# Kernel optimization log

Hardware: AMD Instinct MI355X
Metric: run time of the kernel (lower is better)

The kernel has to match this reference:

```python
import jax, jax.numpy as jnp
import numpy as np

B, H, S, D = 4, 16, 2048, 64


def setup_inputs() -> dict:
    key = jax.random.key(0)
    kq, kk, kv = jax.random.split(key, 3)
    Q = jax.random.normal(kq, (B, H, S, D), dtype=jnp.float32)
    K = jax.random.normal(kk, (B, H, S, D), dtype=jnp.float32)
    V = jax.random.normal(kv, (B, H, S, D), dtype=jnp.float32)
    mask = jnp.ones((1, 1, S, S), dtype=jnp.int32)
    return {"Q": Q, "K": K, "V": V, "mask": mask}


def reference(Q, K, V, mask):
    d_k = Q.shape[-1]
    scale = 1.0 / jnp.sqrt(jnp.asarray(d_k, dtype=Q.dtype))
    # [B, H, S, S] attention scores
    attn = jnp.einsum('bhqd,bhkd->bhqk', Q, K) * scale
    # mask == 0 -> -1e9 (matches torch boolean-index assignment)
    attn = jnp.where(mask == 0, jnp.asarray(-1e9, dtype=attn.dtype), attn)
    softmax_attn = jax.nn.softmax(attn, axis=-1)
    out = jnp.einsum('bhqk,bhkd->bhqd', softmax_attn, V)
    return out
```

## Files before the change

kernel.cpp:

```cpp
#include <hip/hip_runtime.h>

typedef __bf16 bf16;
typedef __attribute__((ext_vector_type(8))) __bf16 bf16x8;
typedef __attribute__((ext_vector_type(8))) ushort ushort8v;
typedef __attribute__((ext_vector_type(4))) ushort ushort4v;
typedef __attribute__((ext_vector_type(2))) uint uint2v;
typedef __attribute__((ext_vector_type(4))) float f32x4;

constexpr int S_LEN = 2048;
constexpr int DH    = 64;
constexpr int KVBLK = 64;
constexpr int NT    = S_LEN / KVBLK;
constexpr int QW    = 64;
constexpr float QSCALE = 0.125f * 1.44269504088896f;
constexpr float NEG    = -1.44269504e9f;
constexpr float THR    = 8.0f;
constexpr size_t TILE_BYTES = (size_t)KVBLK * DH * 2;
constexpr size_t KV_BYTES   = (size_t)64 * NT * TILE_BYTES;

__device__ __forceinline__ ushort bfb(float f) {
  bf16 b = (bf16)f;
  return __builtin_bit_cast(ushort, b);
}
__device__ __forceinline__ int SWZ(int row) {
  return ((row & 7) ^ ((row >> 3) & 7)) << 4;
}
__device__ __forceinline__ uint cvtpk(float lo, float hi) {
  uint r;
  asm("v_cvt_pk_bf16_f32 %0, %1, %2" : "=v"(r) : "v"(lo), "v"(hi));
  return r;
}

__global__ __launch_bounds__(256)
void mask_flags(const int* __restrict__ M, uint* __restrict__ F) {
  const int qt  = blockIdx.x;
  const int kt0 = blockIdx.y * 4;
  const int tid = threadIdx.x;
  const int r  = tid >> 2;
  const int c0 = (tid & 3) * 16;
  __shared__ int s[4];
  uint bits = 0;
  for (int i = 0; i < 4; ++i) {
    const int kt = kt0 + i;
    const int* row = M + (size_t)(qt * 64 + r) * S_LEN + kt * 64 + c0;
    int ok = 1;
#pragma unroll
    for (int j = 0; j < 4; ++j) {
      int4 v = *(const int4*)(row + j * 4);
      ok &= (v.x != 0) & (v.y != 0) & (v.z != 0) & (v.w != 0);
    }
    ok = __all(ok) ? 1 : 0;
    if ((tid & 63) == 0) s[tid >> 6] = ok;
    __syncthreads();
    if (s[0] & s[1] & s[2] & s[3]) bits |= 1u << kt;
    __syncthreads();
  }
  if (tid == 0) atomicOr(&F[qt], bits);
}

__global__ __launch_bounds__(256)
void cvt_kv(const float* __restrict__ K, const float* __restrict__ V,
            char* __restrict__ kws, char* __restrict__ vws) {
  const int t = blockIdx.x, bh = blockIdx.y, tid = threadIdx.x;
  const float* Kb = K + ((size_t)bh * S_LEN + t * KVBLK) * DH;
  const float* Vb = V + ((size_t)bh * S_LEN + t * KVBLK) * DH;
  char* kd = kws + ((size_t)bh * NT + t) * TILE_BYTES;
  char* vd = vws + ((size_t)bh * NT + t) * TILE_BYTES;

  const int kr0 = tid >> 3, kc8 = tid & 7;
#pragma unroll
  for (int h = 0; h < 2; ++h) {
    const int row = kr0 + 32 * h;
    const float* kp = Kb + (size_t)row * DH + kc8 * 8;
    float4 a = *(const float4*)kp;
    float4 b = *(const float4*)(kp + 4);
    ushort8v pk;
    pk[0]=bfb(a.x); pk[1]=bfb(a.y); pk[2]=bfb(a.z); pk[3]=bfb(a.w);
    pk[4]=bfb(b.x); pk[5]=bfb(b.y); pk[6]=bfb(b.z); pk[7]=bfb(b.w);
    *(ushort8v*)(kd + row * 128 + ((kc8 * 16) ^ SWZ(row))) = pk;
  }
  const int vr = (tid >> 4) * 4, vc = (tid & 15) * 4;
  float rr[4][4];
#pragma unroll
  for (int i = 0; i < 4; ++i)
    *(float4*)rr[i] = *(const float4*)(Vb + (size_t)(vr + i) * DH + vc);
#pragma unroll
  for (int c = 0; c < 4; ++c) {
    const int d = vc + c;
    ushort4v p4;
    p4[0]=bfb(rr[0][c]); p4[1]=bfb(rr[1][c]);
    p4[2]=bfb(rr[2][c]); p4[3]=bfb(rr[3][c]);
    *(ushort4v*)(vd + d * 128 + ((vr * 2) ^ SWZ(d))) = p4;
  }
}

__global__ __launch_bounds__(64, 2)
void attn_fwd_direct(const float* __restrict__ Q, const int* __restrict__ M,
                     const uint* __restrict__ F, const char* __restrict__ kws,
                     const char* __restrict__ vws, float* __restrict__ O)
{
  __shared__ __align__(16) uint pbw[QW * 32];

  const int lane = threadIdx.x & 63;
  const int qr   = lane & 15;
  const int kg   = lane >> 4;

  const int bid = blockIdx.x;
  const int nid = (bid & 7) * 256 + (bid >> 3);
  const int q0  = (nid & 31) * QW;
  const int bh  = nid >> 5;

  const float* Qb = Q + (size_t)bh * S_LEN * DH;
  const uint fmask = F[q0 >> 6];

  const char* kbase = kws + (size_t)bh * NT * TILE_BYTES;
  const char* vbase = vws + (size_t)bh * NT * TILE_BYTES;

  bf16x8 qf[4][2];
#pragma unroll
  for (int f = 0; f < 4; ++f) {
    const float* qp = Qb + (size_t)(q0 + f * 16 + qr) * DH + kg * 8;
#pragma unroll
    for (int ks = 0; ks < 2; ++ks) {
      float4 a = *(const float4*)(qp + ks * 32);
      float4 b = *(const float4*)(qp + ks * 32 + 4);
      bf16x8 t2;
      t2[0]=(bf16)(a.x*QSCALE); t2[1]=(bf16)(a.y*QSCALE);
      t2[2]=(bf16)(a.z*QSCALE); t2[3]=(bf16)(a.w*QSCALE);
      t2[4]=(bf16)(b.x*QSCALE); t2[5]=(bf16)(b.y*QSCALE);
      t2[6]=(bf16)(b.z*QSCALE); t2[7]=(bf16)(b.w*QSCALE);
      qf[f][ks] = t2;
    }
  }

  f32x4 acc[4][4];
#pragma unroll
  for (int f = 0; f < 4; ++f)
#pragma unroll
    for (int nt = 0; nt < 4; ++nt) { f32x4 z = {0.f,0.f,0.f,0.f}; acc[f][nt] = z; }
  float mrow[4] = {-1e30f,-1e30f,-1e30f,-1e30f};
  float rsum[4] = {0.f,0.f,0.f,0.f};

  int lofs[4][2];
#pragma unroll
  for (int x = 0; x < 4; ++x) {
    const int row = 16 * x + qr;
    const int sw  = SWZ(row);
#pragma unroll
    for (int ks = 0; ks < 2; ++ks)
      lofs[x][ks] = row * 128 + ((kg * 16 + 64 * ks) ^ sw);
  }
  const int psw = (qr & 7) << 4;

  for (int t = 0; t < NT; ++t) {
    const char* kt = kbase + (size_t)t * TILE_BYTES;
    const char* vt = vbase + (size_t)t * TILE_BYTES;

    f32x4 sc[4][4];
#pragma unroll
    for (int f = 0; f < 4; ++f)
#pragma unroll
      for (int ct = 0; ct < 4; ++ct) { f32x4 z = {0.f,0.f,0.f,0.f}; sc[f][ct] = z; }

    __builtin_amdgcn_s_setprio(1);
#pragma unroll
    for (int ct = 0; ct < 4; ++ct)
#pragma unroll
      for (int ks = 0; ks < 2; ++ks) {
        bf16x8 kf = *(const bf16x8*)(kt + lofs[ct][ks]);
        sc[0][ct] = __builtin_amdgcn_mfma_f32_16x16x32_bf16(kf, qf[0][ks], sc[0][ct], 0,0,0);
        sc[1][ct] = __builtin_amdgcn_mfma_f32_16x16x32_bf16(kf, qf[1][ks], sc[1][ct], 0,0,0);
        sc[2][ct] = __builtin_amdgcn_mfma_f32_16x16x32_bf16(kf, qf[2][ks], sc[2][ct], 0,0,0);
        sc[3][ct] = __builtin_amdgcn_mfma_f32_16x16x32_bf16(kf, qf[3][ks], sc[3][ct], 0,0,0);
      }
    __builtin_amdgcn_s_setprio(0);

    bf16x8 vfr[4][2];
#pragma unroll
    for (int nt = 0; nt < 4; ++nt)
#pragma unroll
      for (int ks = 0; ks < 2; ++ks)
        vfr[nt][ks] = *(const bf16x8*)(vt + lofs[nt][ks]);

    const bool allset = ((fmask >> t) & 1u) != 0u;

#pragma unroll
    for (int f = 0; f < 4; ++f) {
      if (!allset) {
        const size_t mo = (size_t)(q0 + f * 16 + qr) * S_LEN + t * KVBLK + 4 * kg;
#pragma unroll
        for (int ct = 0; ct < 4; ++ct)
#pragma unroll
          for (int r = 0; r < 4; ++r)
            if (M[mo + 16 * ct + r] == 0) sc[f][ct][r] = NEG;
      }

      float a0 = fmaxf(fmaxf(sc[f][0][0], sc[f][0][1]), sc[f][0][2]);
      float a1 = fmaxf(fmaxf(sc[f][0][3], sc[f][1][0]), sc[f][1][1]);
      float a2 = fmaxf(fmaxf(sc[f][1][2], sc[f][1][3]), sc[f][2][0]);
      float a3 = fmaxf(fmaxf(sc[f][2][1], sc[f][2][2]), sc[f][2][3]);
      float a4 = fmaxf(fmaxf(sc[f][3][0], sc[f][3][1]), sc[f][3][2]);
      float lm = fmaxf(fmaxf(a0, a1), a2);
      lm = fmaxf(fmaxf(lm, a3), a4);
      lm = fmaxf(lm, sc[f][3][3]);
      lm = fmaxf(lm, __shfl_xor(lm, 16));
      lm = fmaxf(lm, __shfl_xor(lm, 32));

      if (!__all(lm - mrow[f] <= THR)) {
        const float mnew = fmaxf(mrow[f], lm);
        const float corr = __builtin_amdgcn_exp2f(mrow[f] - mnew);
        rsum[f] *= corr;
#pragma unroll
        for (int nt = 0; nt < 4; ++nt) acc[f][nt] *= corr;
        mrow[f] = mnew;
      }

      float p[4][4];
      float ps = 0.f;
#pragma unroll
      for (int ct = 0; ct < 4; ++ct)
#pragma unroll
        for (int r = 0; r < 4; ++r) {
          p[ct][r] = __builtin_amdgcn_exp2f(sc[f][ct][r] - mrow[f]);
          ps += p[ct][r];
        }
      rsum[f] += ps;

      char* pb = (char*)pbw + (f * 16 + qr) * 128;
#pragma unroll
      for (int ct = 0; ct < 4; ++ct) {
        uint2v d2;
        d2[0] = cvtpk(p[ct][0], p[ct][1]);
        d2[1] = cvtpk(p[ct][2], p[ct][3]);
        *(uint2v*)(pb + ((32 * ct + 8 * kg) ^ psw)) = d2;
      }
    }

    __builtin_amdgcn_s_setprio(1);
#pragma unroll
    for (int ks = 0; ks < 2; ++ks) {
      bf16x8 pf0 = *(const bf16x8*)((char*)pbw + (0 * 16 + qr) * 128 + ((kg * 16 + 64 * ks) ^ psw));
      bf16x8 pf1 = *(const bf16x8*)((char*)pbw + (1 * 16 + qr) * 128 + ((kg * 16 + 64 * ks) ^ psw));
      bf16x8 pf2 = *(const bf16x8*)((char*)pbw + (2 * 16 + qr) * 128 + ((kg * 16 + 64 * ks) ^ psw));
      bf16x8 pf3 = *(const bf16x8*)((char*)pbw + (3 * 16 + qr) * 128 + ((kg * 16 + 64 * ks) ^ psw));
#pragma unroll
      for (int nt = 0; nt < 4; ++nt) {
        bf16x8 vf = vfr[nt][ks];
        acc[0][nt] = __builtin_amdgcn_mfma_f32_16x16x32_bf16(vf, pf0, acc[0][nt], 0,0,0);
        acc[1][nt] = __builtin_amdgcn_mfma_f32_16x16x32_bf16(vf, pf1, acc[1][nt], 0,0,0);
        acc[2][nt] = __builtin_amdgcn_mfma_f32_16x16x32_bf16(vf, pf2, acc[2][nt], 0,0,0);
        acc[3][nt] = __builtin_amdgcn_mfma_f32_16x16x32_bf16(vf, pf3, acc[3][nt], 0,0,0);
      }
    }
    __builtin_amdgcn_s_setprio(0);
  }

#pragma unroll
  for (int f = 0; f < 4; ++f) {
    float rs = rsum[f];
    rs += __shfl_xor(rs, 16);
    rs += __shfl_xor(rs, 32);
    const float inv = 1.0f / rs;
    float* Ob = O + ((size_t)bh * S_LEN + q0 + f * 16 + qr) * DH;
#pragma unroll
    for (int nt = 0; nt < 4; ++nt) {
      float4 o = { acc[f][nt][0] * inv, acc[f][nt][1] * inv,
                   acc[f][nt][2] * inv, acc[f][nt][3] * inv };
      *(float4*)(Ob + 16 * nt + 4 * kg) = o;
    }
  }
}

__global__ __launch_bounds__(256, 4)
void attn_fwd_fb(const float* __restrict__ Q, const float* __restrict__ K,
                 const float* __restrict__ V, const int* __restrict__ M,
                 float* __restrict__ O)
{
  __shared__ __align__(16) ushort kb[KVBLK * DH];
  __shared__ __align__(16) ushort vb[DH * KVBLK];
  __shared__ __align__(16) uint   pbw[4 * 32 * 32];

  const int tid  = threadIdx.x;
  const int lane = tid & 63;
  const int w    = tid >> 6;
  const int qr   = lane & 15;
  const int kg   = lane >> 4;

  const int flat = blockIdx.y * gridDim.x + blockIdx.x;
  const int nid  = (flat & 7) * 128 + (flat >> 3);
  const int q0   = (nid & 15) * 128;
  const int bh   = nid >> 4;

  const float* Qb = Q + ((size_t)bh * S_LEN) * DH;
  const float* Kb = K + ((size_t)bh * S_LEN) * DH;
  const float* Vb = V + ((size_t)bh * S_LEN) * DH;

  bf16x8 qf[2][2];
#pragma unroll
  for (int f = 0; f < 2; ++f) {
    const float* qp = Qb + (size_t)(q0 + w * 32 + f * 16 + qr) * DH + kg * 8;
#pragma unroll
    for (int ks = 0; ks < 2; ++ks) {
      float4 a = *(const float4*)(qp + ks * 32);
      float4 b = *(const float4*)(qp + ks * 32 + 4);
      bf16x8 t2;
      t2[0]=(bf16)(a.x*QSCALE); t2[1]=(bf16)(a.y*QSCALE);
      t2[2]=(bf16)(a.z*QSCALE); t2[3]=(bf16)(a.w*QSCALE);
      t2[4]=(bf16)(b.x*QSCALE); t2[5]=(bf16)(b.y*QSCALE);
      t2[6]=(bf16)(b.z*QSCALE); t2[7]=(bf16)(b.w*QSCALE);
      qf[f][ks] = t2;
    }
  }

  f32x4 acc[2][4];
#pragma unroll
  for (int f = 0; f < 2; ++f)
#pragma unroll
    for (int nt = 0; nt < 4; ++nt) { f32x4 z = {0.f,0.f,0.f,0.f}; acc[f][nt] = z; }
  float mrow[2] = {-1e30f, -1e30f};
  float rsum[2] = {0.f, 0.f};

  int lofs[4][2];
#pragma unroll
  for (int x = 0; x < 4; ++x) {
    const int row = 16 * x + qr;
    const int sw  = SWZ(row);
#pragma unroll
    for (int ks = 0; ks < 2; ++ks)
      lofs[x][ks] = row * 128 + ((kg * 16 + 64 * ks) ^ sw);
  }
  char* pb0 = (char*)pbw + (w * 32 + qr) * 128;
  char* pb1 = pb0 + 16 * 128;
  const int psw = (qr & 7) << 4;

  const int kr0 = tid >> 3, kc8 = tid & 7;
  const int vr = (tid >> 4) * 4, vc = (tid & 15) * 4;

  for (int t = 0; t < NT; ++t) {
    const int kv0 = t * KVBLK;
#pragma unroll
    for (int h = 0; h < 2; ++h) {
      const int row = kr0 + 32 * h;
      const float* kp = Kb + (size_t)(kv0 + row) * DH + kc8 * 8;
      float4 a = *(const float4*)kp;
      float4 b = *(const float4*)(kp + 4);
      ushort8v pk;
      pk[0]=bfb(a.x); pk[1]=bfb(a.y); pk[2]=bfb(a.z); pk[3]=bfb(a.w);
      pk[4]=bfb(b.x); pk[5]=bfb(b.y); pk[6]=bfb(b.z); pk[7]=bfb(b.w);
      *(ushort8v*)((char*)kb + row * 128 + ((kc8 * 16) ^ SWZ(row))) = pk;
    }
    float rr[4][4];
#pragma unroll
    for (int i = 0; i < 4; ++i)
      *(float4*)rr[i] = *(const float4*)(Vb + (size_t)(kv0 + vr + i) * DH + vc);
#pragma unroll
    for (int c = 0; c < 4; ++c) {
      const int d = vc + c;
      ushort4v p4;
      p4[0]=bfb(rr[0][c]); p4[1]=bfb(rr[1][c]);
      p4[2]=bfb(rr[2][c]); p4[3]=bfb(rr[3][c]);
      *(ushort4v*)((char*)vb + d * 128 + ((vr * 2) ^ SWZ(d))) = p4;
    }
    __syncthreads();

    f32x4 sc[2][4];
#pragma unroll
    for (int ct = 0; ct < 4; ++ct) {
      f32x4 z = {0.f,0.f,0.f,0.f};
      sc[0][ct] = z; sc[1][ct] = z;
#pragma unroll
      for (int ks = 0; ks < 2; ++ks) {
        bf16x8 kf = *(const bf16x8*)((const char*)kb + lofs[ct][ks]);
        sc[0][ct] = __builtin_amdgcn_mfma_f32_16x16x32_bf16(kf, qf[0][ks], sc[0][ct], 0,0,0);
        sc[1][ct] = __builtin_amdgcn_mfma_f32_16x16x32_bf16(kf, qf[1][ks], sc[1][ct], 0,0,0);
      }
    }

#pragma unroll
    for (int f = 0; f < 2; ++f) {
      const size_t mo = (size_t)(q0 + w * 32 + f * 16 + qr) * S_LEN + t * KVBLK + 4 * kg;
#pragma unroll
      for (int ct = 0; ct < 4; ++ct)
#pragma unroll
        for (int r = 0; r < 4; ++r)
          if (M[mo + 16 * ct + r] == 0) sc[f][ct][r] = NEG;

      float a0 = fmaxf(fmaxf(sc[f][0][0], sc[f][0][1]), sc[f][0][2]);
      float a1 = fmaxf(fmaxf(sc[f][0][3], sc[f][1][0]), sc[f][1][1]);
      float a2 = fmaxf(fmaxf(sc[f][1][2], sc[f][1][3]), sc[f][2][0]);
      float a3 = fmaxf(fmaxf(sc[f][2][1], sc[f][2][2]), sc[f][2][3]);
      float a4 = fmaxf(fmaxf(sc[f][3][0], sc[f][3][1]), sc[f][3][2]);
      float lm = fmaxf(fmaxf(a0, a1), a2);
      lm = fmaxf(fmaxf(lm, a3), a4);
      lm = fmaxf(lm, sc[f][3][3]);
      lm = fmaxf(lm, __shfl_xor(lm, 16));
      lm = fmaxf(lm, __shfl_xor(lm, 32));

      if (!__all(lm - mrow[f] <= THR)) {
        const float mnew = fmaxf(mrow[f], lm);
        const float corr = __builtin_amdgcn_exp2f(mrow[f] - mnew);
        rsum[f] *= corr;
#pragma unroll
        for (int nt = 0; nt < 4; ++nt) acc[f][nt] *= corr;
        mrow[f] = mnew;
      }

      float p[4][4];
      float ps = 0.f;
#pragma unroll
      for (int ct = 0; ct < 4; ++ct)
#pragma unroll
        for (int r = 0; r < 4; ++r) {
          p[ct][r] = __builtin_amdgcn_exp2f(sc[f][ct][r] - mrow[f]);
          ps += p[ct][r];
        }
      rsum[f] += ps;

      char* pb = f ? pb1 : pb0;
#pragma unroll
      for (int ct = 0; ct < 4; ++ct) {
        uint2v d2;
        d2[0] = cvtpk(p[ct][0], p[ct][1]);
        d2[1] = cvtpk(p[ct][2], p[ct][3]);
        *(uint2v*)(pb + ((32 * ct + 8 * kg) ^ psw)) = d2;
      }
    }

#pragma unroll
    for (int ks = 0; ks < 2; ++ks) {
      bf16x8 pf0 = *(const bf16x8*)(pb0 + ((kg * 16 + 64 * ks) ^ psw));
      bf16x8 pf1 = *(const bf16x8*)(pb1 + ((kg * 16 + 64 * ks) ^ psw));
#pragma unroll
      for (int nt = 0; nt < 4; ++nt) {
        bf16x8 vf = *(const bf16x8*)((const char*)vb + lofs[nt][ks]);
        acc[0][nt] = __builtin_amdgcn_mfma_f32_16x16x32_bf16(vf, pf0, acc[0][nt], 0,0,0);
        acc[1][nt] = __builtin_amdgcn_mfma_f32_16x16x32_bf16(vf, pf1, acc[1][nt], 0,0,0);
      }
    }
    __syncthreads();
  }

#pragma unroll
  for (int f = 0; f < 2; ++f) {
    float rs = rsum[f];
    rs += __shfl_xor(rs, 16);
    rs += __shfl_xor(rs, 32);
    const float inv = 1.0f / rs;
    float* Ob = O + ((size_t)bh * S_LEN + q0 + w * 32 + f * 16 + qr) * DH;
#pragma unroll
    for (int nt = 0; nt < 4; ++nt) {
      float4 o = { acc[f][nt][0] * inv, acc[f][nt][1] * inv,
                   acc[f][nt][2] * inv, acc[f][nt][3] * inv };
      *(float4*)(Ob + 16 * nt + 4 * kg) = o;
    }
  }
}

extern "C" void kernel_launch(void* const* d_in, const int* in_sizes, int n_in,
                              void* d_out, int out_size, void* d_ws, size_t ws_size,
                              hipStream_t stream)
{
  const float* Q = (const float*)d_in[0];
  const float* K = (const float*)d_in[1];
  const float* V = (const float*)d_in[2];
  const int*   M = (const int*)d_in[3];
  float* O = (float*)d_out;

  const size_t need = 4096 + 2 * KV_BYTES;
  const bool pre = (d_ws != nullptr) && (ws_size >= need);

  if (pre) {
    uint* F   = (uint*)d_ws;
    char* kws = (char*)d_ws + 4096;
    char* vws = kws + KV_BYTES;
    hipMemsetAsync(F, 0, 32 * sizeof(uint), stream);
    mask_flags<<<dim3(32, 8), 256, 0, stream>>>(M, F);
    cvt_kv<<<dim3(NT, 64), 256, 0, stream>>>(K, V, kws, vws);
    attn_fwd_direct<<<2048, 64, 0, stream>>>(Q, M, F, kws, vws, O);
  } else {
    attn_fwd_fb<<<dim3(16, 64), 256, 0, stream>>>(Q, K, V, M, O);
  }
}
```

Baseline: 126.4 us.

## Split KV sequence across two waves per block with LDS softmax merge

Each block now runs two wavefronts, each covering half of the KV tiles for the same 64 query rows, so the serial KV loop per wave is half as long. At the end, wave 1 writes its accumulator, row max and row sum to LDS, and wave 0 merges them with rescaled online-softmax correction before writing the output. This doubles the waves in flight for the same grid, at the cost of extra LDS (a second P buffer plus the merge scratch), two block barriers, and merge work done by only one wave.

```diff
diff --git a/kernel.cpp b/kernel.cpp
--- a/kernel.cpp
+++ b/kernel.cpp
@@ -12,6 +12,7 @@
 constexpr int KVBLK = 64;
 constexpr int NT    = S_LEN / KVBLK;
 constexpr int QW    = 64;
+constexpr int HT    = NT / 2;
 constexpr float QSCALE = 0.125f * 1.44269504088896f;
 constexpr float NEG    = -1.44269504e9f;
 constexpr float THR    = 8.0f;
@@ -94,14 +95,17 @@
   }
 }
 
-__global__ __launch_bounds__(64, 2)
+__global__ __launch_bounds__(128, 2)
 void attn_fwd_direct(const float* __restrict__ Q, const int* __restrict__ M,
                      const uint* __restrict__ F, const char* __restrict__ kws,
                      const char* __restrict__ vws, float* __restrict__ O)
 {
-  __shared__ __align__(16) uint pbw[QW * 32];
-
-  const int lane = threadIdx.x & 63;
+  __shared__ __align__(16) uint  pbw[2 * QW * 32];
+  __shared__ float scal[8 * 64];
+
+  const int tid  = threadIdx.x;
+  const int lane = tid & 63;
+  const int w    = tid >> 6;
   const int qr   = lane & 15;
   const int kg   = lane >> 4;
 
@@ -150,9 +154,11 @@
     for (int ks = 0; ks < 2; ++ks)
       lofs[x][ks] = row * 128 + ((kg * 16 + 64 * ks) ^ sw);
   }
+  char* pwave = (char*)pbw + w * QW * 128;
   const int psw = (qr & 7) << 4;
 
-  for (int t = 0; t < NT; ++t) {
+  const int t0 = w * HT;
+  for (int t = t0; t < t0 + HT; ++t) {
     const char* kt = kbase + (size_t)t * TILE_BYTES;
     const char* vt = vbase + (size_t)t * TILE_BYTES;
 
@@ -226,7 +232,7 @@
         }
       rsum[f] += ps;
 
-      char* pb = (char*)pbw + (f * 16 + qr) * 128;
+      char* pb = pwave + (f * 16 + qr) * 128;
 #pragma unroll
       for (int ct = 0; ct < 4; ++ct) {
         uint2v d2;
@@ -239,10 +245,10 @@
     __builtin_amdgcn_s_setprio(1);
 #pragma unroll
     for (int ks = 0; ks < 2; ++ks) {
-      bf16x8 pf0 = *(const bf16x8*)((char*)pbw + (0 * 16 + qr) * 128 + ((kg * 16 + 64 * ks) ^ psw));
-      bf16x8 pf1 = *(const bf16x8*)((char*)pbw + (1 * 16 + qr) * 128 + ((kg * 16 + 64 * ks) ^ psw));
-      bf16x8 pf2 = *(const bf16x8*)((char*)pbw + (2 * 16 + qr) * 128 + ((kg * 16 + 64 * ks) ^ psw));
-      bf16x8 pf3 = *(const bf16x8*)((char*)pbw + (3 * 16 + qr) * 128 + ((kg * 16 + 64 * ks) ^ psw));
+      bf16x8 pf0 = *(const bf16x8*)(pwave + (0 * 16 + qr) * 128 + ((kg * 16 + 64 * ks) ^ psw));
+      bf16x8 pf1 = *(const bf16x8*)(pwave + (1 * 16 + qr) * 128 + ((kg * 16 + 64 * ks) ^ psw));
+      bf16x8 pf2 = *(const bf16x8*)(pwave + (2 * 16 + qr) * 128 + ((kg * 16 + 64 * ks) ^ psw));
+      bf16x8 pf3 = *(const bf16x8*)(pwave + (3 * 16 + qr) * 128 + ((kg * 16 + 64 * ks) ^ psw));
 #pragma unroll
       for (int nt = 0; nt < 4; ++nt) {
         bf16x8 vf = vfr[nt][ks];
@@ -257,16 +263,45 @@
 
 #pragma unroll
   for (int f = 0; f < 4; ++f) {
-    float rs = rsum[f];
-    rs += __shfl_xor(rs, 16);
-    rs += __shfl_xor(rs, 32);
-    const float inv = 1.0f / rs;
-    float* Ob = O + ((size_t)bh * S_LEN + q0 + f * 16 + qr) * DH;
-#pragma unroll
-    for (int nt = 0; nt < 4; ++nt) {
-      float4 o = { acc[f][nt][0] * inv, acc[f][nt][1] * inv,
-                   acc[f][nt][2] * inv, acc[f][nt][3] * inv };
-      *(float4*)(Ob + 16 * nt + 4 * kg) = o;
+    rsum[f] += __shfl_xor(rsum[f], 16);
+    rsum[f] += __shfl_xor(rsum[f], 32);
+  }
+
+  __syncthreads();
+  float* accd = (float*)pbw;
+  if (w == 1) {
+#pragma unroll
+    for (int f = 0; f < 4; ++f) {
+#pragma unroll
+      for (int nt = 0; nt < 4; ++nt)
+#pragma unroll
+        for (int j = 0; j < 4; ++j)
+          accd[(f * 16 + nt * 4 + j) * 64 + lane] = acc[f][nt][j];
+      scal[f * 64 + lane] = mrow[f];
+      scal[(4 + f) * 64 + lane] = rsum[f];
+    }
+  }
+  __syncthreads();
+  if (w == 0) {
+#pragma unroll
+    for (int f = 0; f < 4; ++f) {
+      const float m1  = scal[f * 64 + lane];
+      const float rs1 = scal[(4 + f) * 64 + lane];
+      const float m   = fmaxf(mrow[f], m1);
+      const float c0  = __builtin_amdgcn_exp2f(mrow[f] - m);
+      const float c1  = __builtin_amdgcn_exp2f(m1 - m);
+      const float inv = 1.0f / (rsum[f] * c0 + rs1 * c1);
+      float* Ob = O + ((size_t)bh * S_LEN + q0 + f * 16 + qr) * DH;
+#pragma unroll
+      for (int nt = 0; nt < 4; ++nt) {
+        float4 o;
+#pragma unroll
+        for (int j = 0; j < 4; ++j) {
+          const float a1 = accd[(f * 16 + nt * 4 + j) * 64 + lane];
+          ((float*)&o)[j] = (acc[f][nt][j] * c0 + a1 * c1) * inv;
+        }
+        *(float4*)(Ob + 16 * nt + 4 * kg) = o;
+      }
     }
   }
 }
@@ -476,7 +511,7 @@
     hipMemsetAsync(F, 0, 32 * sizeof(uint), stream);
     mask_flags<<<dim3(32, 8), 256, 0, stream>>>(M, F);
     cvt_kv<<<dim3(NT, 64), 256, 0, stream>>>(K, V, kws, vws);
-    attn_fwd_direct<<<2048, 64, 0, stream>>>(Q, M, F, kws, vws, O);
+    attn_fwd_direct<<<2048, 128, 0, stream>>>(Q, M, F, kws, vws, O);
   } else {
     attn_fwd_fb<<<dim3(16, 64), 256, 0, stream>>>(Q, K, V, M, O);
   }
```

Result: slower. 145.0 us (+14.7%).
